# Optimization experiments

Measured on AMD Instinct MI355X. Metric: run time of the kernel, lower is better.

The kernel has to match this reference:

```python
import jax, jax.numpy as jnp
import numpy as np

KSIZE = 7   # init kernel_size
SIGMA = 1.5  # init sigma (>0, so OpenCV uses the analytic Gaussian formula)

def _gauss_kernel1d(ksize, sigma):
    # Matches cv2.getGaussianKernel for sigma > 0
    xs = np.arange(ksize, dtype=np.float64) - (ksize - 1) / 2.0
    k = np.exp(-(xs ** 2) / (2.0 * sigma ** 2))
    k = k / k.sum()
    return jnp.asarray(k.astype(np.float32))

def setup_inputs() -> dict:
    key = jax.random.key(0)
    x = jax.random.uniform(key, (64, 512, 512, 3), dtype=jnp.float32)
    return {"x": x}

def reference(x):
    # Separable Gaussian blur with BORDER_REFLECT_101 ('reflect') padding,
    # identical math to cv2.GaussianBlur(img, (KSIZE, KSIZE), SIGMA).
    k = _gauss_kernel1d(KSIZE, SIGMA)
    pad = KSIZE // 2
    C = x.shape[-1]
    dn = jax.lax.conv_dimension_numbers(x.shape, (KSIZE, 1, 1, C), ('NHWC', 'HWIO', 'NHWC'))
    # Vertical pass (blur along H)
    xp = jnp.pad(x, ((0, 0), (pad, pad), (0, 0), (0, 0)), mode='reflect')
    kh = jnp.tile(k.reshape(KSIZE, 1, 1, 1), (1, 1, 1, C))  # depthwise kernel
    y = jax.lax.conv_general_dilated(xp, kh, (1, 1), 'VALID',
                                     dimension_numbers=dn, feature_group_count=C)
    # Horizontal pass (blur along W)
    yp = jnp.pad(y, ((0, 0), (0, 0), (pad, pad), (0, 0)), mode='reflect')
    kw = jnp.tile(k.reshape(1, KSIZE, 1, 1), (1, 1, 1, C))
    out = jax.lax.conv_general_dilated(yp, kw, (1, 1), 'VALID',
                                       dimension_numbers=dn, feature_group_count=C)
    return out
```

## Files before the change

### kernel.cpp

```cpp
#include <hip/hip_runtime.h>

namespace {

constexpr int HIMG = 512;
constexpr int ROWF = 512 * 3;
constexpr int NT   = 384;
constexpr int RCH  = 4;
constexpr int NLOAD = RCH + 6;
constexpr int HALO = 12;
constexpr int RP   = HALO + ROWF + HALO;
constexpr int CHUNKS = HIMG / RCH;

typedef float vf4 __attribute__((ext_vector_type(4)));

constexpr double KD0 = 0.13533528323661270;
constexpr double KD1 = 0.41111229050718745;
constexpr double KD2 = 0.80073740291680804;
constexpr double KSUM = 1.0 + 2.0 * (KD0 + KD1 + KD2);

__global__ __launch_bounds__(NT, 6) void gauss7(const float* __restrict__ in,
                                                float* __restrict__ out) {
  constexpr float W[7] = {
      (float)(KD0 / KSUM), (float)(KD1 / KSUM), (float)(KD2 / KSUM),
      (float)(1.0 / KSUM),
      (float)(KD2 / KSUM), (float)(KD1 / KSUM), (float)(KD0 / KSUM)};

  __shared__ __align__(16) float lds[RCH][RP];

  const int bid = blockIdx.x;
  const int b   = (bid & 7) * (CHUNKS * 64 / 8) + (bid >> 3);

  const int n  = b >> 7;
  const int hc = b & 127;
  const int h0 = hc * RCH;
  const int t  = threadIdx.x;

  const float* inN  = in  + (size_t)n * HIMG * ROWF;
  float*       outN = out + (size_t)n * HIMG * ROWF;
  const float4* inCol = reinterpret_cast<const float4*>(inN) + t;

  float4 rw[NLOAD];
#pragma unroll
  for (int i = 0; i < NLOAD; ++i) {
    int r  = h0 - 3 + i;
    int rr = r < 0 ? -r : (r > HIMG - 1 ? 2 * (HIMG - 1) - r : r);
    rw[i]  = inCol[(size_t)rr * NT];
  }

#pragma unroll
  for (int i = 0; i < RCH; ++i) {
    float4 v;
    v.x = W[0]*rw[i].x + W[1]*rw[i+1].x + W[2]*rw[i+2].x + W[3]*rw[i+3].x +
          W[4]*rw[i+4].x + W[5]*rw[i+5].x + W[6]*rw[i+6].x;
    v.y = W[0]*rw[i].y + W[1]*rw[i+1].y + W[2]*rw[i+2].y + W[3]*rw[i+3].y +
          W[4]*rw[i+4].y + W[5]*rw[i+5].y + W[6]*rw[i+6].y;
    v.z = W[0]*rw[i].z + W[1]*rw[i+1].z + W[2]*rw[i+2].z + W[3]*rw[i+3].z +
          W[4]*rw[i+4].z + W[5]*rw[i+5].z + W[6]*rw[i+6].z;
    v.w = W[0]*rw[i].w + W[1]*rw[i+1].w + W[2]*rw[i+2].w + W[3]*rw[i+3].w +
          W[4]*rw[i+4].w + W[5]*rw[i+5].w + W[6]*rw[i+6].w;

    float* lrow = &lds[i][HALO];
    *reinterpret_cast<float4*>(lrow + 4 * t) = v;

    if (t == 0) {
      lrow[-3] = v.w;
    } else if (t == 1) {
      lrow[-2] = v.x; lrow[-1] = v.y; lrow[-6] = v.z; lrow[-5] = v.w;
    } else if (t == 2) {
      lrow[-4] = v.x; lrow[-9] = v.y; lrow[-8] = v.z; lrow[-7] = v.w;
    } else if (t == NT - 3) {
      lrow[1542] = v.x; lrow[1543] = v.y; lrow[1544] = v.z; lrow[1539] = v.w;
    } else if (t == NT - 2) {
      lrow[1540] = v.x; lrow[1541] = v.y; lrow[1536] = v.z; lrow[1537] = v.w;
    } else if (t == NT - 1) {
      lrow[1538] = v.x;
    }
  }
  __syncthreads();

#pragma unroll
  for (int k = 0; k < RCH; ++k) {
    const float* rowp = &lds[k][HALO + 4 * t - 12];
    float s[28];
#pragma unroll
    for (int j = 0; j < 7; ++j)
      *reinterpret_cast<float4*>(&s[4 * j]) =
          *reinterpret_cast<const float4*>(rowp + 4 * j);
    vf4 o;
#pragma unroll
    for (int m = 0; m < 4; ++m)
      o[m] = W[0]*s[m+3]  + W[1]*s[m+6]  + W[2]*s[m+9]  + W[3]*s[m+12] +
             W[4]*s[m+15] + W[5]*s[m+18] + W[6]*s[m+21];
    vf4* orow = reinterpret_cast<vf4*>(outN + (size_t)(h0 + k) * ROWF);
    __builtin_nontemporal_store(o, orow + t);
  }
}

}

extern "C" void kernel_launch(void* const* d_in, const int* in_sizes, int n_in,
                              void* d_out, int out_size, void* d_ws, size_t ws_size,
                              hipStream_t stream) {
  const float* x = (const float*)d_in[0];
  float*       y = (float*)d_out;
  dim3 grid(64 * CHUNKS);
  dim3 block(NT);
  hipLaunchKernelGGL(gauss7, grid, block, 0, stream, x, y);
}
```

Measured before the change: 62.84 us.

## Restructure blur as per-wave column strips with rolling vertical window

Each wavefront now owns a 256-float span of a 32-row strip. It streams rows with a one-row prefetch, does the horizontal pass first through a per-wave LDS row (halo lanes load the reflected edges), and keeps a rolling 7-row register window for the vertical pass. This cuts the vertical halo overread from 10 loads per 4 output rows to 38 per 32 rows and replaces block-wide barriers with wave-local LDS use. The cost is less parallelism per block, a serial row loop with per-row LDS round trips, and scalar halo loads.

```diff
diff --git a/kernel.cpp b/kernel.cpp
--- a/kernel.cpp
+++ b/kernel.cpp
@@ -3,13 +3,12 @@
 namespace {
 
 constexpr int HIMG = 512;
-constexpr int ROWF = 512 * 3;
-constexpr int NT   = 384;
-constexpr int RCH  = 4;
-constexpr int NLOAD = RCH + 6;
-constexpr int HALO = 12;
-constexpr int RP   = HALO + ROWF + HALO;
-constexpr int CHUNKS = HIMG / RCH;
+constexpr int ROWF = 1536;
+constexpr int SH   = 32;
+constexpr int SPANS = 6;
+constexpr int STRIPS = HIMG / SH;
+constexpr int LROW = 288;
+constexpr int WPB  = 4;
 
 typedef float vf4 __attribute__((ext_vector_type(4)));
 
@@ -18,81 +17,102 @@
 constexpr double KD2 = 0.80073740291680804;
 constexpr double KSUM = 1.0 + 2.0 * (KD0 + KD1 + KD2);
 
-__global__ __launch_bounds__(NT, 6) void gauss7(const float* __restrict__ in,
-                                                float* __restrict__ out) {
+__device__ __forceinline__ int reflect_f(int f) {
+  int c = f % 3; if (c < 0) c += 3;
+  int p = (f - c) / 3;
+  p = p < 0 ? -p : (p > 511 ? 1022 - p : p);
+  return 3 * p + c;
+}
+
+__global__ __launch_bounds__(64 * WPB, 6) void gauss7(const float* __restrict__ in,
+                                                      float* __restrict__ out) {
   constexpr float W[7] = {
       (float)(KD0 / KSUM), (float)(KD1 / KSUM), (float)(KD2 / KSUM),
       (float)(1.0 / KSUM),
       (float)(KD2 / KSUM), (float)(KD1 / KSUM), (float)(KD0 / KSUM)};
 
-  __shared__ __align__(16) float lds[RCH][RP];
+  __shared__ __align__(16) float lds[WPB][LROW];
 
   const int bid = blockIdx.x;
-  const int b   = (bid & 7) * (CHUNKS * 64 / 8) + (bid >> 3);
+  const int b   = (bid & 7) * 192 + (bid >> 3);
 
-  const int n  = b >> 7;
-  const int hc = b & 127;
-  const int h0 = hc * RCH;
-  const int t  = threadIdx.x;
+  const int wid  = threadIdx.x >> 6;
+  const int lane = threadIdx.x & 63;
+  const int gw   = b * WPB + wid;
+  const int img  = gw / (SPANS * STRIPS);
+  const int rem  = gw - img * (SPANS * STRIPS);
+  const int span = rem >> 4;
+  const int strip= rem & 15;
+  const int h0   = strip * SH;
+  const int spanf= span << 8;
 
-  const float* inN  = in  + (size_t)n * HIMG * ROWF;
-  float*       outN = out + (size_t)n * HIMG * ROWF;
-  const float4* inCol = reinterpret_cast<const float4*>(inN) + t;
+  const float* inN  = in  + (size_t)img * HIMG * ROWF;
+  float*       outN = out + (size_t)img * HIMG * ROWF;
+  float* wrow = lds[wid];
 
-  float4 rw[NLOAD];
-#pragma unroll
-  for (int i = 0; i < NLOAD; ++i) {
-    int r  = h0 - 3 + i;
-    int rr = r < 0 ? -r : (r > HIMG - 1 ? 2 * (HIMG - 1) - r : r);
-    rw[i]  = inCol[(size_t)rr * NT];
+  const int ownf = spanf + 4 * lane;
+
+  const bool hact = (lane < 3) || (lane >= 61);
+  int ldsoff = 0, sf0 = 0, sf1 = 0, sf2 = 0, sf3 = 0;
+  if (lane < 3) {
+    ldsoff = 4 * lane;
+    const int f = spanf - 12 + 4 * lane;
+    sf0 = reflect_f(f);     sf1 = reflect_f(f + 1);
+    sf2 = reflect_f(f + 2); sf3 = reflect_f(f + 3);
+  } else if (lane >= 61) {
+    ldsoff = 268 + 4 * (lane - 61);
+    const int f = spanf + 256 + 4 * (lane - 61);
+    sf0 = reflect_f(f);     sf1 = reflect_f(f + 1);
+    sf2 = reflect_f(f + 2); sf3 = reflect_f(f + 3);
   }
 
-#pragma unroll
-  for (int i = 0; i < RCH; ++i) {
-    float4 v;
-    v.x = W[0]*rw[i].x + W[1]*rw[i+1].x + W[2]*rw[i+2].x + W[3]*rw[i+3].x +
-          W[4]*rw[i+4].x + W[5]*rw[i+5].x + W[6]*rw[i+6].x;
-    v.y = W[0]*rw[i].y + W[1]*rw[i+1].y + W[2]*rw[i+2].y + W[3]*rw[i+3].y +
-          W[4]*rw[i+4].y + W[5]*rw[i+5].y + W[6]*rw[i+6].y;
-    v.z = W[0]*rw[i].z + W[1]*rw[i+1].z + W[2]*rw[i+2].z + W[3]*rw[i+3].z +
-          W[4]*rw[i+4].z + W[5]*rw[i+5].z + W[6]*rw[i+6].z;
-    v.w = W[0]*rw[i].w + W[1]*rw[i+1].w + W[2]*rw[i+2].w + W[3]*rw[i+3].w +
-          W[4]*rw[i+4].w + W[5]*rw[i+5].w + W[6]*rw[i+6].w;
+  auto loadrow = [&](int r, float4& own, float4& hal) {
+    const int rr = r < 0 ? -r : (r > 511 ? 1022 - r : r);
+    const float* rp = inN + (size_t)rr * ROWF;
+    own = *reinterpret_cast<const float4*>(rp + ownf);
+    if (hact) {
+      hal.x = rp[sf0]; hal.y = rp[sf1]; hal.z = rp[sf2]; hal.w = rp[sf3];
+    }
+  };
 
-    float* lrow = &lds[i][HALO];
-    *reinterpret_cast<float4*>(lrow + 4 * t) = v;
+  float4 win0{}, win1{}, win2{}, win3{}, win4{}, win5{};
+  float4 curo, curh{}, nxto, nxth{};
+  loadrow(h0 - 3, curo, curh);
 
-    if (t == 0) {
-      lrow[-3] = v.w;
-    } else if (t == 1) {
-      lrow[-2] = v.x; lrow[-1] = v.y; lrow[-6] = v.z; lrow[-5] = v.w;
-    } else if (t == 2) {
-      lrow[-4] = v.x; lrow[-9] = v.y; lrow[-8] = v.z; lrow[-7] = v.w;
-    } else if (t == NT - 3) {
-      lrow[1542] = v.x; lrow[1543] = v.y; lrow[1544] = v.z; lrow[1539] = v.w;
-    } else if (t == NT - 2) {
-      lrow[1540] = v.x; lrow[1541] = v.y; lrow[1536] = v.z; lrow[1537] = v.w;
-    } else if (t == NT - 1) {
-      lrow[1538] = v.x;
-    }
-  }
-  __syncthreads();
+  const int rlast = h0 + SH + 2;
+  for (int r = h0 - 3; r <= rlast; ++r) {
+    if (r < rlast) loadrow(r + 1, nxto, nxth);
 
-#pragma unroll
-  for (int k = 0; k < RCH; ++k) {
-    const float* rowp = &lds[k][HALO + 4 * t - 12];
+    *reinterpret_cast<float4*>(wrow + 12 + 4 * lane) = curo;
+    if (hact) *reinterpret_cast<float4*>(wrow + ldsoff) = curh;
+    asm volatile("" ::: "memory");
+
     float s[28];
 #pragma unroll
     for (int j = 0; j < 7; ++j)
       *reinterpret_cast<float4*>(&s[4 * j]) =
-          *reinterpret_cast<const float4*>(rowp + 4 * j);
-    vf4 o;
-#pragma unroll
-    for (int m = 0; m < 4; ++m)
-      o[m] = W[0]*s[m+3]  + W[1]*s[m+6]  + W[2]*s[m+9]  + W[3]*s[m+12] +
-             W[4]*s[m+15] + W[5]*s[m+18] + W[6]*s[m+21];
-    vf4* orow = reinterpret_cast<vf4*>(outN + (size_t)(h0 + k) * ROWF);
-    __builtin_nontemporal_store(o, orow + t);
+          *reinterpret_cast<const float4*>(wrow + 4 * lane + 4 * j);
+    float4 hb;
+    hb.x = W[0]*s[3] + W[1]*s[6] + W[2]*s[9]  + W[3]*s[12] + W[4]*s[15] + W[5]*s[18] + W[6]*s[21];
+    hb.y = W[0]*s[4] + W[1]*s[7] + W[2]*s[10] + W[3]*s[13] + W[4]*s[16] + W[5]*s[19] + W[6]*s[22];
+    hb.z = W[0]*s[5] + W[1]*s[8] + W[2]*s[11] + W[3]*s[14] + W[4]*s[17] + W[5]*s[20] + W[6]*s[23];
+    hb.w = W[0]*s[6] + W[1]*s[9] + W[2]*s[12] + W[3]*s[15] + W[4]*s[18] + W[5]*s[21] + W[6]*s[24];
+
+    if (r >= h0 + 3) {
+      vf4 o;
+      o[0] = W[0]*win0.x + W[1]*win1.x + W[2]*win2.x + W[3]*win3.x +
+             W[4]*win4.x + W[5]*win5.x + W[6]*hb.x;
+      o[1] = W[0]*win0.y + W[1]*win1.y + W[2]*win2.y + W[3]*win3.y +
+             W[4]*win4.y + W[5]*win5.y + W[6]*hb.y;
+      o[2] = W[0]*win0.z + W[1]*win1.z + W[2]*win2.z + W[3]*win3.z +
+             W[4]*win4.z + W[5]*win5.z + W[6]*hb.z;
+      o[3] = W[0]*win0.w + W[1]*win1.w + W[2]*win2.w + W[3]*win3.w +
+             W[4]*win4.w + W[5]*win5.w + W[6]*hb.w;
+      vf4* orow = reinterpret_cast<vf4*>(outN + (size_t)(r - 3) * ROWF + spanf);
+      __builtin_nontemporal_store(o, orow + lane);
+    }
+    win0 = win1; win1 = win2; win2 = win3; win3 = win4; win4 = win5; win5 = hb;
+    curo = nxto; curh = nxth;
   }
 }
 
@@ -103,7 +123,7 @@
                               hipStream_t stream) {
   const float* x = (const float*)d_in[0];
   float*       y = (float*)d_out;
-  dim3 grid(64 * CHUNKS);
-  dim3 block(NT);
+  dim3 grid(64 * SPANS * STRIPS / WPB);
+  dim3 block(64 * WPB);
   hipLaunchKernelGGL(gauss7, grid, block, 0, stream, x, y);
 }
```

Result: slower. 78.90 us (+25.6%).
